# Performance work log

Hardware: AMD Instinct MI355X
Metric: run time of the kernel (lower is better)

## Reference

```python
import jax, jax.numpy as jnp
import numpy as np
from jax import lax

D_MODEL = 1024
N_HEADS = 16
KERNEL = 3
STRIDE = 1
PAD = 1
BATCH = 32
SEQ = D_MODEL  # required by the module's reshape: seq_len must equal d_model


def setup_inputs() -> dict:
    key = jax.random.key(0)
    k1, k2, k3, k4, k5, k6 = jax.random.split(key, 6)
    query_sequences = jax.random.normal(k1, (BATCH, SEQ, D_MODEL), dtype=jnp.float32)
    key_sequences = jax.random.normal(k2, (BATCH, SEQ, D_MODEL), dtype=jnp.float32)
    value_sequences = jax.random.normal(k3, (BATCH, SEQ, D_MODEL), dtype=jnp.float32)
    key_value_sequence_lengths = jax.random.randint(k4, (BATCH,), 0, SEQ).astype(jnp.int64)
    # nn.Linear(d_model, n_heads*kernel_size) params (stored as (in, out) for x @ W)
    scale = 1.0 / np.sqrt(D_MODEL)
    Wq = jax.random.uniform(k5, (D_MODEL, N_HEADS * KERNEL), minval=-scale, maxval=scale, dtype=jnp.float32)
    bq = jax.random.uniform(k6, (N_HEADS * KERNEL,), minval=-scale, maxval=scale, dtype=jnp.float32)
    return {
        "query_sequences": query_sequences,
        "key_sequences": key_sequences,
        "value_sequences": value_sequences,
        "key_value_sequence_lengths": key_value_sequence_lengths,
        "Wq": Wq,
        "bq": bq,
    }


def reference(query_sequences, key_sequences, value_sequences, key_value_sequence_lengths, Wq, bq):
    B, S, D = query_sequences.shape
    # per-batch dynamic conv kernels from queries: (B, S, H*K) -> (B*H, D, K)
    # (valid because S == D, mirroring the torch .view)
    qk = jnp.einsum('bsd,df->bsf', query_sequences, Wq) + bq
    kernels = qk.reshape(B * N_HEADS, D, KERNEL)
    # keys as a single grouped-conv input: (1, B*D, S)
    keys = jnp.transpose(key_sequences, (0, 2, 1)).reshape(1, B * D, S)
    # grouped conv1d with groups = batch_size (each group: in=D, out=N_HEADS)
    out = lax.conv_general_dilated(
        keys, kernels,
        window_strides=(STRIDE,),
        padding=[(PAD, PAD)],
        dimension_numbers=('NCH', 'OIH', 'NCH'),
        feature_group_count=B,
    )
    return out.reshape(B, N_HEADS, S)
```

## Files before the change

### kernel.cpp

```cpp
#include <hip/hip_runtime.h>
#include <hip/hip_bf16.h>
#include <stdint.h>

typedef __attribute__((ext_vector_type(8))) short bf16x8;
typedef __attribute__((ext_vector_type(4))) float f32x4;

__device__ __forceinline__ short f2bf(float x) {
    __hip_bfloat16 h = __float2bfloat16(x);
    return __builtin_bit_cast(short, h);
}

__device__ __forceinline__ bf16x8 pack8(f32x4 a, f32x4 b) {
    bf16x8 r;
    r[0] = f2bf(a[0]); r[1] = f2bf(a[1]); r[2] = f2bf(a[2]); r[3] = f2bf(a[3]);
    r[4] = f2bf(b[0]); r[5] = f2bf(b[1]); r[6] = f2bf(b[2]); r[7] = f2bf(b[3]);
    return r;
}

__global__ __launch_bounds__(256) void prep_wfrag(const float* __restrict__ Wq,
                                                  short* __restrict__ wfrag) {
    int idx = blockIdx.x * 256 + threadIdx.x;
    int j    = idx & 7;
    int lane = (idx >> 3) & 63;
    int grp  = idx >> 9;
    int nf   = grp % 3;
    int ks   = grp / 3;
    int k = ks * 32 + ((lane >> 4) << 3) + j;
    int n = nf * 16 + (lane & 15);
    wfrag[idx] = f2bf(Wq[k * 48 + n]);
}

__global__ __launch_bounds__(256) void qk_gemm(const float* __restrict__ Q,
                                               const short* __restrict__ wfrag,
                                               const float* __restrict__ bq,
                                               short* __restrict__ wgtA) {
    const int l  = threadIdx.x & 63;
    const int w  = threadIdx.x >> 6;
    const int lr = l & 15;
    const int lk = l >> 4;
    const int row0 = blockIdx.x * 64 + w * 16;

    f32x4 acc[3];
    acc[0] = (f32x4){0.f, 0.f, 0.f, 0.f};
    acc[1] = acc[0];
    acc[2] = acc[0];

    const float* qbase = Q + (size_t)(row0 + lr) * 1024 + lk * 8;

    #pragma unroll 4
    for (int ks = 0; ks < 32; ++ks) {
        const float* p = qbase + ks * 32;
        f32x4 q0 = *(const f32x4*)p;
        f32x4 q1 = *(const f32x4*)(p + 4);
        bf16x8 a = pack8(q0, q1);
        const bf16x8* wp = (const bf16x8*)(wfrag + (size_t)ks * 1536 + l * 8);
        acc[0] = __builtin_amdgcn_mfma_f32_16x16x32_bf16(a, wp[0],   acc[0], 0, 0, 0);
        acc[1] = __builtin_amdgcn_mfma_f32_16x16x32_bf16(a, wp[64],  acc[1], 0, 0, 0);
        acc[2] = __builtin_amdgcn_mfma_f32_16x16x32_bf16(a, wp[128], acc[2], 0, 0, 0);
    }

    #pragma unroll
    for (int nf = 0; nf < 3; ++nf) {
        int n = nf * 16 + lr;
        float bias = bq[n];
        int t  = n / 3;
        int kk = n - t * 3;
        #pragma unroll
        for (int r = 0; r < 4; ++r) {
            int row = row0 + lk * 4 + r;
            int b   = row >> 10;
            int h   = (row >> 6) & 15;
            int sp  = row & 63;
            int dg  = sp * 2 + (t >> 3);
            int j   = t & 7;
            wgtA[(((size_t)(b * 3 + kk) * 128 + dg) << 7) + h * 8 + j] = f2bf(acc[nf][r] + bias);
        }
    }
}

__global__ __launch_bounds__(256, 6) void conv_mfma(const float* __restrict__ Key,
                                                    const short* __restrict__ wgtA,
                                                    float* __restrict__ out) {
    __shared__ short klds[2][66][72];
    const int blk = blockIdx.x;
    const int kc  = blk & 3;
    const int st  = (blk >> 2) & 15;
    const int b   = blk >> 6;
    const int s0  = st << 6;
    const int tid = threadIdx.x;
    const int l   = tid & 63;
    const int w   = tid >> 6;
    const int lr  = l & 15;
    const int lk  = l >> 4;

    const float* keyB = Key + ((size_t)b << 20) + (kc << 8);
    const short* wgtW = wgtA + (((size_t)b * 384 + (kc << 5)) << 7) + lk * 128 + lr * 8;

    const int j8 = tid & 7;
    const int r0 = tid >> 3;
    const int srow0 = s0 - 1 + r0;
    const int srow1 = s0 + 31 + r0;
    const int srow2 = s0 + 63 + r0;
    const bool ok0 = (srow0 >= 0);
    const bool ok2 = (tid < 16) && (srow2 < 1024);
    const f32x4* q0 = (const f32x4*)(keyB + (size_t)(ok0 ? srow0 : 0) * 1024 + j8 * 8);
    const f32x4* q1 = (const f32x4*)(keyB + (size_t)srow1 * 1024 + j8 * 8);
    const f32x4* q2 = (const f32x4*)(keyB + (size_t)(ok2 ? srow2 : 0) * 1024 + j8 * 8);

    const f32x4 z4 = (f32x4){0.f, 0.f, 0.f, 0.f};

    {
        f32x4 a0 = ok0 ? q0[0] : z4, a1 = ok0 ? q0[1] : z4;
        f32x4 b0 = q1[0],            b1 = q1[1];
        f32x4 c0 = ok2 ? q2[0] : z4, c1 = ok2 ? q2[1] : z4;
        *(bf16x8*)&klds[0][r0][j8 * 8]      = pack8(a0, a1);
        *(bf16x8*)&klds[0][r0 + 32][j8 * 8] = pack8(b0, b1);
        if (tid < 16) *(bf16x8*)&klds[0][64 + r0][j8 * 8] = pack8(c0, c1);
    }
    __syncthreads();

    f32x4 acc = z4;

    #pragma unroll
    for (int c = 0; c < 4; ++c) {
        const int buf = c & 1;
        const bool pre = (c + 1 < 4);
        f32x4 a0, a1, b0, b1, c0, c1;
        if (pre) {
            const int o = (c + 1) * 16;
            a0 = ok0 ? q0[o] : z4;  a1 = ok0 ? q0[o + 1] : z4;
            b0 = q1[o];             b1 = q1[o + 1];
            c0 = ok2 ? q2[o] : z4;  c1 = ok2 ? q2[o + 1] : z4;
        }
        #pragma unroll
        for (int k = 0; k < 3; ++k) {
            #pragma unroll
            for (int d2 = 0; d2 < 2; ++d2) {
                bf16x8 a  = *(const bf16x8*)(wgtW + (size_t)k * 16384 + (c * 8 + d2 * 4) * 128);
                bf16x8 kv = *(const bf16x8*)(&klds[buf][w * 16 + lr + k][d2 * 32 + lk * 8]);
                acc = __builtin_amdgcn_mfma_f32_16x16x32_bf16(a, kv, acc, 0, 0, 0);
            }
        }
        if (pre) {
            bf16x8 wA = pack8(a0, a1);
            bf16x8 wB = pack8(b0, b1);
            bf16x8 wC = pack8(c0, c1);
            __syncthreads();
            *(bf16x8*)&klds[buf ^ 1][r0][j8 * 8]      = wA;
            *(bf16x8*)&klds[buf ^ 1][r0 + 32][j8 * 8] = wB;
            if (tid < 16) *(bf16x8*)&klds[buf ^ 1][64 + r0][j8 * 8] = wC;
            __syncthreads();
        }
    }

    const int s = s0 + w * 16 + lr;
    #pragma unroll
    for (int r = 0; r < 4; ++r) {
        int h = lk * 4 + r;
        atomicAdd(&out[(((b << 4) + h) << 10) + s], acc[r]);
    }
}

extern "C" void kernel_launch(void* const* d_in, const int* in_sizes, int n_in,
                              void* d_out, int out_size, void* d_ws, size_t ws_size,
                              hipStream_t stream) {
    const float* Q  = (const float*)d_in[0];
    const float* K  = (const float*)d_in[1];
    const float* Wq = (const float*)d_in[4];
    const float* bq = (const float*)d_in[5];
    float* outp = (float*)d_out;

    short* wfrag = (short*)d_ws;
    short* wgtA  = (short*)((char*)d_ws + 98304);

    hipMemsetAsync(outp, 0, (size_t)out_size * sizeof(float), stream);
    hipLaunchKernelGGL(prep_wfrag, dim3(192),  dim3(256), 0, stream, Wq, wfrag);
    hipLaunchKernelGGL(qk_gemm,    dim3(512),  dim3(256), 0, stream, Q, wfrag, bq, wgtA);
    hipLaunchKernelGGL(conv_mfma,  dim3(2048), dim3(256), 0, stream, K, wgtA, outp);
}
```

Measured before the change: 66.44 us.

## Restructure conv kernel to split full d-range in-block and drop atomics and memset

Each conv block now covers 32 sequence positions over the full 1024 channel dimension instead of 64 positions over a quarter of it. The four waves split into two sequence halves and two channel halves, and the channel halves are reduced through shared memory before a plain store. This removes the output memset launch and the global atomicAdds. The LDS tile uses an XOR swizzle to avoid bank conflicts. The cost is a longer serial loop per block, half as many blocks, and a lower occupancy hint.

```diff
diff --git a/kernel.cpp b/kernel.cpp
--- a/kernel.cpp
+++ b/kernel.cpp
@@ -78,86 +78,110 @@
     }
 }
 
-__global__ __launch_bounds__(256, 6) void conv_mfma(const float* __restrict__ Key,
+__global__ __launch_bounds__(256, 4) void conv_mfma(const float* __restrict__ Key,
                                                     const short* __restrict__ wgtA,
                                                     float* __restrict__ out) {
-    __shared__ short klds[2][66][72];
+    __shared__ short klds[2][34][128];
+    __shared__ float red[2][16][17];
     const int blk = blockIdx.x;
-    const int kc  = blk & 3;
-    const int st  = (blk >> 2) & 15;
-    const int b   = blk >> 6;
-    const int s0  = st << 6;
+    const int st  = blk & 31;
+    const int b   = blk >> 5;
+    const int s0  = st << 5;
     const int tid = threadIdx.x;
     const int l   = tid & 63;
     const int w   = tid >> 6;
     const int lr  = l & 15;
     const int lk  = l >> 4;
-
-    const float* keyB = Key + ((size_t)b << 20) + (kc << 8);
-    const short* wgtW = wgtA + (((size_t)b * 384 + (kc << 5)) << 7) + lk * 128 + lr * 8;
-
-    const int j8 = tid & 7;
-    const int r0 = tid >> 3;
-    const int srow0 = s0 - 1 + r0;
-    const int srow1 = s0 + 31 + r0;
-    const int srow2 = s0 + 63 + r0;
-    const bool ok0 = (srow0 >= 0);
-    const bool ok2 = (tid < 16) && (srow2 < 1024);
-    const f32x4* q0 = (const f32x4*)(keyB + (size_t)(ok0 ? srow0 : 0) * 1024 + j8 * 8);
-    const f32x4* q1 = (const f32x4*)(keyB + (size_t)srow1 * 1024 + j8 * 8);
-    const f32x4* q2 = (const f32x4*)(keyB + (size_t)(ok2 ? srow2 : 0) * 1024 + j8 * 8);
+    const int ss  = w & 1;
+    const int dh  = w >> 1;
+
+    const int jg = tid & 15;
+    const int r  = tid >> 4;
+    const int dcol = ((jg & 7) << 3) + ((jg >> 3) << 9);
+    const float* keyB = Key + ((size_t)b << 20) + dcol;
+
+    const bool g0 = (s0 - 1 + r) >= 0;
+    const bool g2 = (r < 2) && (s0 + 31 + r < 1024);
+    const float* p0 = keyB + (size_t)(g0 ? s0 - 1 + r : 0) * 1024;
+    const float* p1 = keyB + (size_t)(s0 + 15 + r) * 1024;
+    const float* p2 = keyB + (size_t)(g2 ? s0 + 31 + r : 0) * 1024;
+
+    const int row0 = r, row1 = r + 16, row2 = r + 32;
+    char* ldsB = (char*)&klds[0][0][0];
+
+    #define STB(buf, row, v) \
+        *(bf16x8*)(ldsB + ((buf) * 34 + (row)) * 256 + ((jg * 16) ^ (((row) & 7) << 4))) = (v)
 
     const f32x4 z4 = (f32x4){0.f, 0.f, 0.f, 0.f};
-
-    {
-        f32x4 a0 = ok0 ? q0[0] : z4, a1 = ok0 ? q0[1] : z4;
-        f32x4 b0 = q1[0],            b1 = q1[1];
-        f32x4 c0 = ok2 ? q2[0] : z4, c1 = ok2 ? q2[1] : z4;
-        *(bf16x8*)&klds[0][r0][j8 * 8]      = pack8(a0, a1);
-        *(bf16x8*)&klds[0][r0 + 32][j8 * 8] = pack8(b0, b1);
-        if (tid < 16) *(bf16x8*)&klds[0][64 + r0][j8 * 8] = pack8(c0, c1);
-    }
+    f32x4 a0, a1, b0, b1, c0, c1;
+
+    a0 = g0 ? p0[0] : 0.f, a0 = g0 ? *(const f32x4*)p0 : z4;
+    a1 = g0 ? *(const f32x4*)(p0 + 4) : z4;
+    b0 = *(const f32x4*)p1;       b1 = *(const f32x4*)(p1 + 4);
+    c0 = g2 ? *(const f32x4*)p2 : z4;
+    c1 = g2 ? *(const f32x4*)(p2 + 4) : z4;
+    STB(0, row0, pack8(a0, a1));
+    STB(0, row1, pack8(b0, b1));
+    if (r < 2) STB(0, row2, pack8(c0, c1));
+    a0 = g0 ? *(const f32x4*)(p0 + 64) : z4;
+    a1 = g0 ? *(const f32x4*)(p0 + 68) : z4;
+    b0 = *(const f32x4*)(p1 + 64);  b1 = *(const f32x4*)(p1 + 68);
+    c0 = g2 ? *(const f32x4*)(p2 + 64) : z4;
+    c1 = g2 ? *(const f32x4*)(p2 + 68) : z4;
     __syncthreads();
 
+    const short* wgtW = wgtA + (((size_t)b * 384 + (dh << 6) + lk) << 7) + lr * 8;
+
     f32x4 acc = z4;
 
     #pragma unroll
-    for (int c = 0; c < 4; ++c) {
-        const int buf = c & 1;
-        const bool pre = (c + 1 < 4);
-        f32x4 a0, a1, b0, b1, c0, c1;
-        if (pre) {
-            const int o = (c + 1) * 16;
-            a0 = ok0 ? q0[o] : z4;  a1 = ok0 ? q0[o + 1] : z4;
-            b0 = q1[o];             b1 = q1[o + 1];
-            c0 = ok2 ? q2[o] : z4;  c1 = ok2 ? q2[o + 1] : z4;
-        }
+    for (int t = 0; t < 8; ++t) {
+        const int buf = t & 1;
         #pragma unroll
         for (int k = 0; k < 3; ++k) {
+            const int row = ss * 16 + lr + k;
+            const char* rb = ldsB + (buf * 34 + row) * 256;
+            const int sw = ((row & 7) << 4);
             #pragma unroll
-            for (int d2 = 0; d2 < 2; ++d2) {
-                bf16x8 a  = *(const bf16x8*)(wgtW + (size_t)k * 16384 + (c * 8 + d2 * 4) * 128);
-                bf16x8 kv = *(const bf16x8*)(&klds[buf][w * 16 + lr + k][d2 * 32 + lk * 8]);
+            for (int kk = 0; kk < 2; ++kk) {
+                bf16x8 kv = *(const bf16x8*)(rb + ((((dh << 7) + (kk << 6) + (lk << 4))) ^ sw));
+                bf16x8 a  = *(const bf16x8*)(wgtW + k * 16384 + t * 1024 + kk * 512);
                 acc = __builtin_amdgcn_mfma_f32_16x16x32_bf16(a, kv, acc, 0, 0, 0);
             }
         }
-        if (pre) {
+        if (t < 7) {
             bf16x8 wA = pack8(a0, a1);
             bf16x8 wB = pack8(b0, b1);
             bf16x8 wC = pack8(c0, c1);
             __syncthreads();
-            *(bf16x8*)&klds[buf ^ 1][r0][j8 * 8]      = wA;
-            *(bf16x8*)&klds[buf ^ 1][r0 + 32][j8 * 8] = wB;
-            if (tid < 16) *(bf16x8*)&klds[buf ^ 1][64 + r0][j8 * 8] = wC;
+            STB(buf ^ 1, row0, wA);
+            STB(buf ^ 1, row1, wB);
+            if (r < 2) STB(buf ^ 1, row2, wC);
+            if (t < 6) {
+                const int o = (t + 2) << 6;
+                a0 = g0 ? *(const f32x4*)(p0 + o) : z4;
+                a1 = g0 ? *(const f32x4*)(p0 + o + 4) : z4;
+                b0 = *(const f32x4*)(p1 + o);  b1 = *(const f32x4*)(p1 + o + 4);
+                c0 = g2 ? *(const f32x4*)(p2 + o) : z4;
+                c1 = g2 ? *(const f32x4*)(p2 + o + 4) : z4;
+            }
             __syncthreads();
         }
     }
-
-    const int s = s0 + w * 16 + lr;
-    #pragma unroll
-    for (int r = 0; r < 4; ++r) {
-        int h = lk * 4 + r;
-        atomicAdd(&out[(((b << 4) + h) << 10) + s], acc[r]);
+    #undef STB
+
+    if (dh == 1) {
+        #pragma unroll
+        for (int r4 = 0; r4 < 4; ++r4) red[ss][lk * 4 + r4][lr] = acc[r4];
+    }
+    __syncthreads();
+    if (dh == 0) {
+        const int s = s0 + ss * 16 + lr;
+        #pragma unroll
+        for (int r4 = 0; r4 < 4; ++r4) {
+            int h = lk * 4 + r4;
+            out[(((b << 4) + h) << 10) + s] = acc[r4] + red[ss][h][lr];
+        }
     }
 }
 
@@ -173,8 +197,7 @@
     short* wfrag = (short*)d_ws;
     short* wgtA  = (short*)((char*)d_ws + 98304);
 
-    hipMemsetAsync(outp, 0, (size_t)out_size * sizeof(float), stream);
     hipLaunchKernelGGL(prep_wfrag, dim3(192),  dim3(256), 0, stream, Wq, wfrag);
     hipLaunchKernelGGL(qk_gemm,    dim3(512),  dim3(256), 0, stream, Q, wfrag, bq, wgtA);
-    hipLaunchKernelGGL(conv_mfma,  dim3(2048), dim3(256), 0, stream, K, wgtA, outp);
-}
+    hipLaunchKernelGGL(conv_mfma,  dim3(1024), dim3(256), 0, stream, K, wgtA, outp);
+}
```

New measurement: 65.63 us. About the same (-1.2%).
